# Kernel optimization log

Measured on AMD Instinct MI355X. Metric: run time of the kernel, lower is better.

## Reference

```python
import jax, jax.numpy as jnp
import numpy as np

NUM_HEADS = 8
N_WIN = 7
TOPK = 4


def _grid2seq(x, rs, m):
    # x: (B, C, H, W) -> (B, m, nregion, reg_size, head_dim)
    B, C, H, W = x.shape
    rh, rw = H // rs[0], W // rs[1]
    d = C // m
    x = x.reshape(B, m, d, rh, rs[0], rw, rs[1])
    x = jnp.einsum('bmdhpwq->bmhwpqd', x).reshape(B, m, rh * rw, rs[0] * rs[1], d)
    return x, rh, rw


def _seq2grid(x, rh, rw, rs):
    B, m, nreg, rsq, d = x.shape
    x = x.reshape(B, m, rh, rw, rs[0], rs[1], d)
    return jnp.einsum('bmhwpqd->bmdhpwq', x).reshape(B, m * d, rh * rs[0], rw * rs[1])


def setup_inputs() -> dict:
    key = jax.random.key(0)
    ks = jax.random.split(key, 7)
    C = 256
    inp = {
        'x': jax.random.normal(ks[0], (16, C, 56, 56), jnp.float32),
        'w_qkv': jax.random.normal(ks[1], (3 * C, C), jnp.float32) * 0.02,
        'b_qkv': jax.random.normal(ks[2], (3 * C,), jnp.float32) * 0.02,
        'w_lepe': jax.random.normal(ks[3], (C, 1, 3, 3), jnp.float32) * 0.02,
        'b_lepe': jax.random.normal(ks[4], (C,), jnp.float32) * 0.02,
        'w_out': jax.random.normal(ks[5], (C, C), jnp.float32) * 0.02,
        'b_out': jax.random.normal(ks[6], (C,), jnp.float32) * 0.02,
    }
    return inp


def reference(x, w_qkv, b_qkv, w_lepe, b_lepe, w_out, b_out):
    N, C, H, W = x.shape
    m = NUM_HEADS
    d = C // m
    scale = d ** (-0.5)
    rs = (max(1, H // N_WIN), max(1, W // N_WIN))  # (8, 8) here; H,W divisible -> no pad
    rh, rw = H // rs[0], W // rs[1]

    # 1x1 conv qkv projection
    qkv = jnp.einsum('nchw,oc->nohw', x, w_qkv) + b_qkv[None, :, None, None]
    q, k, v = jnp.split(qkv, 3, axis=1)

    # region-level routing (avg_pool over each region; exact divisibility -> plain mean)
    def region_mean(t):
        return t.reshape(N, C, rh, rs[0], rw, rs[1]).mean(axis=(3, 5))  # (N,C,rh,rw)

    q_r = jax.lax.stop_gradient(region_mean(q)).reshape(N, C, rh * rw).transpose(0, 2, 1)  # (N,nreg,C)
    k_r = jax.lax.stop_gradient(region_mean(k)).reshape(N, C, rh * rw)  # (N,C,nreg)
    a_r = q_r @ k_r  # (N, nreg, nreg)
    k_fixed = min(TOPK, a_r.shape[-1])
    _, idx_r = jax.lax.top_k(a_r, k_fixed)  # (N, nreg, topk)
    idx_r = jnp.broadcast_to(idx_r[:, None], (N, m, rh * rw, k_fixed))  # (N,m,nreg,topk)

    # token-level attention within routed regions
    q_seq, _, _ = _grid2seq(q, rs, m)  # (N,m,nreg,rs2,d)
    k_seq, _, _ = _grid2seq(k, rs, m)
    v_seq, _, _ = _grid2seq(v, rs, m)
    rs2 = k_seq.shape[-2]

    gather = jax.vmap(jax.vmap(lambda seq, i: seq[i]))  # over (batch, head)
    key_g = gather(k_seq, idx_r).reshape(N, m, rh * rw, k_fixed * rs2, d)
    val_g = gather(v_seq, idx_r).reshape(N, m, rh * rw, k_fixed * rs2, d)

    attn = jax.nn.softmax(jnp.einsum('bmnpd,bmnkd->bmnpk', q_seq * scale, key_g), axis=-1)
    out = jnp.einsum('bmnpk,bmnkd->bmnpd', attn, val_g)
    out = _seq2grid(out, rh, rw, rs)  # (N, C, H, W)

    # LEPE: depthwise 3x3 conv on v
    lepe = jax.lax.conv_general_dilated(
        v, w_lepe, window_strides=(1, 1), padding='SAME',
        feature_group_count=C, dimension_numbers=('NCHW', 'OIHW', 'NCHW'))
    out = out + lepe + b_lepe[None, :, None, None]

    # 1x1 conv output projection
    out = jnp.einsum('nchw,oc->nohw', out, w_out) + b_out[None, :, None, None]
    return out
```

## Files before the change

### kernel.cpp

```cpp
#include <hip/hip_runtime.h>
#include <cstdint>

#define DEV __device__ __forceinline__

using short8 = __attribute__((ext_vector_type(8))) short;
using f32x4  = __attribute__((ext_vector_type(4))) float;

#define MFMA __builtin_amdgcn_mfma_f32_16x16x32_bf16

DEV float bf2f(unsigned short u){
  union { unsigned int i; float f; } v; v.i = ((unsigned int)u) << 16; return v.f;
}
DEV unsigned short f2bf(float f){
  union { float f; unsigned int i; } v; v.f = f;
  unsigned int x = v.i;
  return (unsigned short)((x + 0x7fffu + ((x >> 16) & 1u)) >> 16);
}
DEV unsigned int cvtpk(float a, float b){
  unsigned int r;
  asm("v_cvt_pk_bf16_f32 %0, %1, %2" : "=v"(r) : "v"(a), "v"(b));
  return r;
}

__global__ __launch_bounds__(256) void k_prep(const float* __restrict__ w_qkv,
                                              const float* __restrict__ w_out,
                                              unsigned short* __restrict__ wqh_t,
                                              unsigned short* __restrict__ woh_t,
                                              unsigned short* __restrict__ wol_t){
  int i = blockIdx.x*256 + threadIdx.x;
  if (i < 196608){
    int o = i >> 8, c = i & 255, kc = c >> 5, kk = c & 31;
    wqh_t[kc*24576 + o*32 + kk] = f2bf(w_qkv[i]);
  } else {
    int j = i - 196608;
    if (j < 65536){
      int o = j >> 8, c = j & 255, kc = c >> 5, kk = c & 31;
      float v = w_out[j];
      unsigned short h = f2bf(v);
      int dst = kc*8192 + o*32 + kk;
      woh_t[dst] = h;
      wol_t[dst] = f2bf(v - bf2f(h));
    }
  }
}

__global__ __launch_bounds__(256) void k_xbar(const float* __restrict__ x,
                                              float* __restrict__ xbar){
  const int ry = blockIdx.x, n = blockIdx.y, cz = blockIdx.z;
  const int t = threadIdx.x, cg = t>>6, lane = t&63;
  for (int ci = 0; ci < 16; ++ci){
    int c = cz*64 + ci*4 + cg;
    const float* base = x + ((size_t)n*256 + c)*3136 + ry*8*56;
    float acc = 0.f;
    if (lane < 56){
      #pragma unroll
      for (int yy = 0; yy < 8; ++yy) acc += base[yy*56 + lane];
    }
    acc += __shfl_xor(acc, 1, 64);
    acc += __shfl_xor(acc, 2, 64);
    acc += __shfl_xor(acc, 4, 64);
    if ((lane&7) == 0 && lane < 56)
      xbar[((size_t)n*49 + ry*7 + (lane>>3))*256 + c] = acc * (1.0f/64.0f);
  }
}

__global__ __launch_bounds__(256) void k_qrkr(const float* __restrict__ xbar,
                                              const float* __restrict__ w_qkv,
                                              const float* __restrict__ b_qkv,
                                              float* __restrict__ q_r,
                                              float* __restrict__ k_r){
  __shared__ float4 xb4[448];
  const int wb = blockIdx.x, n = blockIdx.y, rz = blockIdx.z, t = threadIdx.x;
  {
    const float4* src = (const float4*)(xbar + (size_t)n*12544) + rz*448;
    for (int i = t; i < 448; i += 256) xb4[i] = src[i];
  }
  const int wrow = wb*64 + (t>>2), kl = t&3;
  float4 wreg[16];
  {
    const float4* wsrc = (const float4*)(w_qkv + (size_t)wrow*256) + kl*16;
    #pragma unroll
    for (int i = 0; i < 16; ++i) wreg[i] = wsrc[i];
  }
  __syncthreads();
  const float bias = b_qkv[wrow];
  for (int rl = 0; rl < 7; ++rl){
    float s = 0.f;
    #pragma unroll
    for (int i = 0; i < 16; ++i){
      float4 a = wreg[i], b = xb4[rl*64 + kl*16 + i];
      s += a.x*b.x + a.y*b.y + a.z*b.z + a.w*b.w;
    }
    s += __shfl_xor(s, 1, 64);
    s += __shfl_xor(s, 2, 64);
    if (kl == 0){
      int reg = rz*7 + rl;
      if (wrow < 256) q_r[((size_t)n*49 + reg)*256 + wrow] = s + bias;
      else            k_r[((size_t)n*49 + reg)*256 + wrow - 256] = s + bias;
    }
  }
}

__global__ __launch_bounds__(64) void k_topk(const float* __restrict__ q_r,
                                             const float* __restrict__ k_r,
                                             int* __restrict__ idx){
  __shared__ float sc[49];
  const int qreg = blockIdx.x, n = blockIdx.y, l = threadIdx.x;
  const float* qrow = q_r + ((size_t)n*49 + qreg)*256;
  const float q0 = qrow[l], q1 = qrow[l+64], q2 = qrow[l+128], q3 = qrow[l+192];
  for (int kr = 0; kr < 49; ++kr){
    const float* krow = k_r + ((size_t)n*49 + kr)*256;
    float s = q0*krow[l] + q1*krow[l+64] + q2*krow[l+128] + q3*krow[l+192];
    #pragma unroll
    for (int m = 1; m < 64; m <<= 1) s += __shfl_xor(s, m, 64);
    if (l == 0) sc[kr] = s;
  }
  __syncthreads();
  if (l == 0){
    #pragma unroll
    for (int s = 0; s < 4; ++s){
      float best = -3.4e38f; int bi = 0;
      for (int kr = 0; kr < 49; ++kr) if (sc[kr] > best){ best = sc[kr]; bi = kr; }
      idx[((size_t)n*49 + qreg)*4 + s] = bi;
      sc[bi] = -3.4e38f;
    }
  }
}

__global__ __launch_bounds__(256) void k_qkv(const float* __restrict__ x,
                                             const unsigned short* __restrict__ wqh_t,
                                             const float* __restrict__ b_qkv,
                                             unsigned short* __restrict__ q_rm,
                                             unsigned short* __restrict__ k_rm,
                                             unsigned short* __restrict__ v_t){
  __shared__ unsigned short xl[64*256];
  const int lin = blockIdx.x;
  const int xcd = lin & 7, jj = lin >> 3;
  const int jobid = xcd*294 + jj;
  const int z = jobid % 3;
  const int pair = jobid / 3;
  const int reg = pair % 49, n = pair / 49;

  const int ry = reg/7, rx = reg%7;
  const int t = threadIdx.x, w = t>>6, g = (t>>4)&3, c16 = t&15;
  {
    const int pq = (t & 15)*4, cc = t >> 4;
    const int row = pq >> 3, col = pq & 7;
    const float* src = x + ((size_t)n*256 + cc)*3136 + (ry*8 + row)*56 + rx*8 + col;
    for (int ci = 0; ci < 16; ++ci){
      float4 v4 = *reinterpret_cast<const float4*>(src + (size_t)ci*16*3136);
      int c = ci*16 + cc;
      xl[((pq+0)*256 + c) ^ (((pq+0)&15)<<3)] = f2bf(v4.x);
      xl[((pq+1)*256 + c) ^ (((pq+1)&15)<<3)] = f2bf(v4.y);
      xl[((pq+2)*256 + c) ^ (((pq+2)&15)<<3)] = f2bf(v4.z);
      xl[((pq+3)*256 + c) ^ (((pq+3)&15)<<3)] = f2bf(v4.w);
    }
  }
  __syncthreads();
  const size_t rb = (size_t)(n*8)*49 + reg;
  const int osw = w*16;

  if (z < 2){
    f32x4 acc[4][4] = {};
    for (int kc = 0; kc < 8; ++kc){
      short8 xf[4];
      #pragma unroll
      for (int pt = 0; pt < 4; ++pt){
        int p = pt*16 + c16;
        xf[pt] = *reinterpret_cast<const short8*>(&xl[(p*256 + kc*32 + 8*g) ^ ((p&15)<<3)]);
      }
      #pragma unroll
      for (int oi = 0; oi < 4; ++oi){
        const int os = z*256 + oi*64 + osw;
        short8 wf = *reinterpret_cast<const short8*>(wqh_t + (size_t)kc*24576 + (os + c16)*32 + 8*g);
        #pragma unroll
        for (int pt = 0; pt < 4; ++pt)
          acc[oi][pt] = MFMA(xf[pt], wf, acc[oi][pt], 0, 0, 0);
      }
    }
    #pragma unroll
    for (int oi = 0; oi < 4; ++oi){
      const int o = z*256 + oi*64 + osw + c16;
      const float bias = b_qkv[o];
      const int oc = o & 255, hh = oc >> 5, dd = oc & 31;
      unsigned short* dst = ((z == 0) ? q_rm : k_rm) + (rb + hh*49)*2048 + dd;
      #pragma unroll
      for (int pt = 0; pt < 4; ++pt)
        #pragma unroll
        for (int r = 0; r < 4; ++r){
          int tok = pt*16 + 4*g + r;
          dst[tok*32] = f2bf(acc[oi][pt][r] + bias);
        }
    }
  } else {
    f32x4 acc[4][4] = {};
    for (int kc = 0; kc < 8; ++kc){
      short8 xf[4];
      #pragma unroll
      for (int pt = 0; pt < 4; ++pt){
        int p = pt*16 + c16;
        xf[pt] = *reinterpret_cast<const short8*>(&xl[(p*256 + kc*32 + 8*g) ^ ((p&15)<<3)]);
      }
      #pragma unroll
      for (int oi = 0; oi < 4; ++oi){
        const int os = oi*64 + osw;
        short8 wf = *reinterpret_cast<const short8*>(wqh_t + (size_t)kc*24576 + (512 + os + c16)*32 + 8*g);
        #pragma unroll
        for (int pt = 0; pt < 4; ++pt)
          acc[oi][pt] = MFMA(wf, xf[pt], acc[oi][pt], 0, 0, 0);
      }
    }
    #pragma unroll
    for (int oi = 0; oi < 4; ++oi){
      #pragma unroll
      for (int r = 0; r < 4; ++r){
        int c = oi*64 + osw + 4*g + r;
        const float bias = b_qkv[512 + c];
        int hh = c >> 5, ch = c & 31;
        unsigned short* dst = v_t + (rb + hh*49)*2048 + ch*32;
        #pragma unroll
        for (int pt = 0; pt < 4; ++pt){
          int tok = pt*16 + c16;
          dst[(tok>>5)*1024 + (tok&31)] = f2bf(acc[oi][pt][r] + bias);
        }
      }
    }
  }
}

__global__ __launch_bounds__(256, 4) void k_attn(const unsigned short* __restrict__ q_rm,
                                                 const unsigned short* __restrict__ k_rm,
                                                 const unsigned short* __restrict__ v_t,
                                                 const int* __restrict__ idx,
                                                 const float* __restrict__ w_lepe,
                                                 const float* __restrict__ b_lepe,
                                                 unsigned short* __restrict__ att_hi,
                                                 unsigned short* __restrict__ att_lo){
  __shared__ unsigned short halo[10*320];
  __shared__ float wl_s[288];
  __shared__ float bl_s[32];

  const int lin = blockIdx.x + 49*(blockIdx.y + 8*blockIdx.z);
  const int xcd = lin & 7, j = lin >> 3;
  const int jq = j / 49;
  const int qreg = j - jq*49;
  const int hn = jq*8 + xcd;
  const int h = hn & 7, n = hn >> 3;

  const int t = threadIdx.x, w = t>>6, g = (t>>4)&3, c16 = t&15;
  const int ry = qreg/7, rx = qreg%7;
  const int gy0 = ry*8;

  int4 ridx = *reinterpret_cast<const int4*>(idx + ((size_t)n*49 + qreg)*4);
  int regs[4] = {ridx.x, ridx.y, ridx.z, ridx.w};

  const size_t hb = ((size_t)(n*8 + h))*49;

  wl_s[t < 288 ? t : 0] = w_lepe[h*288 + (t < 288 ? t : 0)];
  if (t < 32){
    wl_s[256 + t] = w_lepe[h*288 + 256 + t];
    bl_s[t] = b_lepe[h*32 + t];
  }
  #pragma unroll
  for (int pass = 0; pass < 2; ++pass){
    int s = pass ? (256 + t) : t;
    if (pass == 0 || t < 64){
      const int dy = s >> 5, c = s & 31;
      const int yy = gy0 + dy - 1;
      short8 inner = {0,0,0,0,0,0,0,0};
      unsigned short eL = 0, eR = 0;
      if (yy >= 0 && yy < 56){
        const int iry = yy >> 3, y7 = yy & 7;
        const size_t rowb = (size_t)(y7>>2)*1024 + c*32 + (y7&3)*8;
        inner = *reinterpret_cast<const short8*>(v_t + (hb + iry*7 + rx)*2048 + rowb);
        if (rx > 0) eL = v_t[(hb + iry*7 + rx - 1)*2048 + rowb + 7];
        if (rx < 6) eR = v_t[(hb + iry*7 + rx + 1)*2048 + rowb];
      }
      unsigned short* drow = &halo[dy*320 + c*10];
      drow[0] = eL;
      #pragma unroll
      for (int jj2 = 0; jj2 < 8; ++jj2) drow[1 + jj2] = (unsigned short)inner[jj2];
      drow[9] = eR;
    }
  }

  const int qtok = w*16 + c16;
  short8 qf = *reinterpret_cast<const short8*>(q_rm + (hb + qreg)*2048 + qtok*32 + 8*g);

  f32x4 s_acc[16];
  __builtin_amdgcn_s_setprio(1);
  #pragma unroll
  for (int f = 0; f < 16; ++f){
    const int tt = (f&3)*16 + c16;
    short8 kf = *reinterpret_cast<const short8*>(
        k_rm + (hb + regs[f>>2])*2048 + tt*32 + 8*g);
    f32x4 z = {0.f, 0.f, 0.f, 0.f};
    s_acc[f] = MFMA(kf, qf, z, 0, 0, 0);
  }
  __builtin_amdgcn_s_setprio(0);

  const float scale2 = 0.1767766952966369f * 1.4426950408889634f;
  float m = -3.4e38f;
  #pragma unroll
  for (int f = 0; f < 16; ++f)
    #pragma unroll
    for (int r = 0; r < 4; ++r) m = fmaxf(m, s_acc[f][r]);
  m = fmaxf(m, __shfl_xor(m, 16, 64));
  m = fmaxf(m, __shfl_xor(m, 32, 64));
  const float nms = -m*scale2;
  float su = 0.f;
  #pragma unroll
  for (int f = 0; f < 16; ++f)
    #pragma unroll
    for (int r = 0; r < 4; ++r){
      float e = exp2f(fmaf(s_acc[f][r], scale2, nms));
      s_acc[f][r] = e; su += e;
    }
  su += __shfl_xor(su, 16, 64);
  su += __shfl_xor(su, 32, 64);
  const float inv_lane = __builtin_amdgcn_rcpf(su);

  f32x4 oacc[2] = {};
  const int srcA = (t & 15) | ((t & 16) << 1);
  const int srcB = srcA + 16;
  const bool gsel = (t & 32) != 0;
  #pragma unroll
  for (int tc = 0; tc < 8; ++tc){
    const int fb = (tc>>1)*4 + (tc&1)*2;
    unsigned int a0 = cvtpk(s_acc[fb][0],   s_acc[fb][1]);
    unsigned int a1 = cvtpk(s_acc[fb][2],   s_acc[fb][3]);
    unsigned int b0 = cvtpk(s_acc[fb+1][0], s_acc[fb+1][1]);
    unsigned int b1 = cvtpk(s_acc[fb+1][2], s_acc[fb+1][3]);
    unsigned int wa0 = __shfl((int)a0, srcA, 64), wa1 = __shfl((int)a1, srcA, 64);
    unsigned int wa2 = __shfl((int)a0, srcB, 64), wa3 = __shfl((int)a1, srcB, 64);
    unsigned int wb0 = __shfl((int)b0, srcA, 64), wb1 = __shfl((int)b1, srcA, 64);
    unsigned int wb2 = __shfl((int)b0, srcB, 64), wb3 = __shfl((int)b1, srcB, 64);
    union { unsigned int u[4]; short8 s8; } pfu;
    pfu.u[0] = gsel ? wb0 : wa0;
    pfu.u[1] = gsel ? wb1 : wa1;
    pfu.u[2] = gsel ? wb2 : wa2;
    pfu.u[3] = gsel ? wb3 : wa3;
    const size_t vb = (hb + regs[tc>>1])*2048 + (tc&1)*1024 + 8*g;
    __builtin_amdgcn_s_setprio(1);
    #pragma unroll
    for (int dt = 0; dt < 2; ++dt){
      short8 vf = *reinterpret_cast<const short8*>(v_t + vb + (dt*16 + c16)*32);
      oacc[dt] = MFMA(pfu.s8, vf, oacc[dt], 0, 0, 0);
    }
    __builtin_amdgcn_s_setprio(0);
  }

  float invq[4];
  #pragma unroll
  for (int r = 0; r < 4; ++r)
    invq[r] = __shfl(inv_lane, 4*g + r, 64);

  __syncthreads();
  const int tok0 = w*16 + 4*g;
  const int ty = tok0>>3, tx0 = tok0&7;
  #pragma unroll
  for (int dt = 0; dt < 2; ++dt){
    const int cl = dt*16 + c16;
    float wl[9];
    #pragma unroll
    for (int kk = 0; kk < 9; ++kk) wl[kk] = wl_s[cl*9 + kk];
    const float bl = bl_s[cl];
    float vwin[3][6];
    #pragma unroll
    for (int dy = 0; dy < 3; ++dy){
      const unsigned short* hrow = &halo[(ty+dy)*320 + cl*10 + tx0];
      #pragma unroll
      for (int jj = 0; jj < 6; ++jj)
        vwin[dy][jj] = bf2f(hrow[jj]);
    }
    #pragma unroll
    for (int r = 0; r < 4; ++r){
      float a = fmaf(oacc[dt][r], invq[r], bl);
      #pragma unroll
      for (int dy = 0; dy < 3; ++dy)
        #pragma unroll
        for (int dx = 0; dx < 3; ++dx)
          a += wl[dy*3 + dx] * vwin[dy][r + dx];
      int tok = tok0 + r;
      size_t o = ((size_t)(n*49 + qreg)*8 + h)*2048 + tok*32 + dt*16 + c16;
      unsigned short hi = (unsigned short)cvtpk(a, a);
      att_hi[o] = hi;
      float alo = a - bf2f(hi);
      att_lo[o] = (unsigned short)cvtpk(alo, alo);
    }
  }
}

__global__ __launch_bounds__(512) void k_oproj(const unsigned short* __restrict__ ah_,
                                               const unsigned short* __restrict__ al_,
                                               const unsigned short* __restrict__ wh_t,
                                               const unsigned short* __restrict__ wl_t,
                                               const float* __restrict__ b_out,
                                               float* __restrict__ out){
  const int lin = blockIdx.x;
  const int jobid = (lin & 7)*98 + (lin >> 3);
  const int reg = jobid % 49, n = jobid / 49;
  const int t = threadIdx.x, w8 = t>>6, g = (t>>4)&3, c16 = t&15;
  const int ry = reg/7, rx = reg%7;
  const size_t abase = ((size_t)(n*49 + reg))*8*2048;
  const int os1 = w8*16, os2 = os1 + 128;
  f32x4 acc[2][4] = {};
  for (int kc = 0; kc < 8; ++kc){
    const size_t wb = (size_t)kc*8192 + 8*g;
    short8 wh1 = *reinterpret_cast<const short8*>(wh_t + wb + (os1 + c16)*32);
    short8 wl1 = *reinterpret_cast<const short8*>(wl_t + wb + (os1 + c16)*32);
    short8 wh2 = *reinterpret_cast<const short8*>(wh_t + wb + (os2 + c16)*32);
    short8 wl2 = *reinterpret_cast<const short8*>(wl_t + wb + (os2 + c16)*32);
    #pragma unroll
    for (int pt = 0; pt < 4; ++pt){
      size_t off = abase + (size_t)kc*2048 + (pt*16 + c16)*32 + 8*g;
      short8 xh = *reinterpret_cast<const short8*>(ah_ + off);
      short8 xl = *reinterpret_cast<const short8*>(al_ + off);
      acc[0][pt] = MFMA(wh1, xh, acc[0][pt], 0, 0, 0);
      acc[0][pt] = MFMA(wh1, xl, acc[0][pt], 0, 0, 0);
      acc[0][pt] = MFMA(wl1, xh, acc[0][pt], 0, 0, 0);
      acc[1][pt] = MFMA(wh2, xh, acc[1][pt], 0, 0, 0);
      acc[1][pt] = MFMA(wh2, xl, acc[1][pt], 0, 0, 0);
      acc[1][pt] = MFMA(wl2, xh, acc[1][pt], 0, 0, 0);
    }
  }
  #pragma unroll
  for (int s = 0; s < 2; ++s){
    const int os = s ? os2 : os1;
    #pragma unroll
    for (int r = 0; r < 4; ++r){
      int o = os + 4*g + r;
      float bias = b_out[o];
      #pragma unroll
      for (int pt = 0; pt < 4; ++pt){
        int tok = pt*16 + c16;
        int p = (ry*8 + (tok>>3))*56 + rx*8 + (tok&7);
        out[((size_t)n*256 + o)*3136 + p] = acc[s][pt][r] + bias;
      }
    }
  }
}

extern "C" void kernel_launch(void* const* d_in, const int* in_sizes, int n_in,
                              void* d_out, int out_size, void* d_ws, size_t ws_size,
                              hipStream_t stream){
  const float* x      = (const float*)d_in[0];
  const float* w_qkv  = (const float*)d_in[1];
  const float* b_qkv  = (const float*)d_in[2];
  const float* w_lepe = (const float*)d_in[3];
  const float* b_lepe = (const float*)d_in[4];
  const float* w_out  = (const float*)d_in[5];
  const float* b_out  = (const float*)d_in[6];
  float* out = (float*)d_out;

  char* ws = (char*)d_ws;
  size_t off = 0;
  auto take = [&](size_t bytes)->char*{
    char* p = ws + off; off += (bytes + 255) & ~(size_t)255; return p;
  };
  const size_t TEN = (size_t)16*3136*256*2;
  unsigned short* q_rm   = (unsigned short*)take(TEN);
  unsigned short* k_rm   = (unsigned short*)take(TEN);
  unsigned short* v_t    = (unsigned short*)take(TEN);
  unsigned short* att_hi = (unsigned short*)take(TEN);
  unsigned short* att_lo = (unsigned short*)take(TEN);
  float* xbar = (float*)take((size_t)16*49*256*4);
  float* q_r  = (float*)take((size_t)16*49*256*4);
  float* k_r  = (float*)take((size_t)16*49*256*4);
  int*   idxb = (int*)take((size_t)16*49*4*4);
  unsigned short* wqh_t = (unsigned short*)take((size_t)768*256*2);
  unsigned short* woh_t = (unsigned short*)take((size_t)256*256*2);
  unsigned short* wol_t = (unsigned short*)take((size_t)256*256*2);

  k_prep <<<dim3(1024), 256, 0, stream>>>(w_qkv, w_out, wqh_t, woh_t, wol_t);
  k_xbar <<<dim3(7, 16, 4), 256, 0, stream>>>(x, xbar);
  k_qrkr <<<dim3(8, 16, 7), 256, 0, stream>>>(xbar, w_qkv, b_qkv, q_r, k_r);
  k_topk <<<dim3(49, 16), 64, 0, stream>>>(q_r, k_r, idxb);
  k_qkv  <<<dim3(2352), 256, 0, stream>>>(x, wqh_t, b_qkv, q_rm, k_rm, v_t);
  k_attn <<<dim3(49, 8, 16), 256, 0, stream>>>(q_rm, k_rm, v_t, idxb, w_lepe, b_lepe, att_hi, att_lo);
  k_oproj<<<dim3(784), 512, 0, stream>>>(att_hi, att_lo, woh_t, wol_t, b_out, out);
}
```

Before: 248.9 us.

## Fuse routed attention and output projection into one kernel via LDS staging

Merges the attention+LEPE kernel and the output projection kernel into a single kernel that runs one block per (batch, region). Each of the 8 waves handles one head and loops over four query tiles. The hi/lo bf16 attention result is packed into shared memory and consumed directly by the projection MFMAs. This removes the global round trip of the att_hi/att_lo buffers and one kernel launch. In exchange the grid shrinks to 784 blocks with large LDS use (about 116KB) and a launch bound of one block per CU, which reduces occupancy and latency hiding.

After: 256.6 us. 1.03x slower.

```diff
diff --git a/kernel.cpp b/kernel.cpp
--- a/kernel.cpp
+++ b/kernel.cpp
@@ -228,182 +228,166 @@
   }
 }
 
-__global__ __launch_bounds__(256, 4) void k_attn(const unsigned short* __restrict__ q_rm,
-                                                 const unsigned short* __restrict__ k_rm,
-                                                 const unsigned short* __restrict__ v_t,
-                                                 const int* __restrict__ idx,
-                                                 const float* __restrict__ w_lepe,
-                                                 const float* __restrict__ b_lepe,
-                                                 unsigned short* __restrict__ att_hi,
-                                                 unsigned short* __restrict__ att_lo){
-  __shared__ unsigned short halo[10*320];
-  __shared__ float wl_s[288];
-  __shared__ float bl_s[32];
-
-  const int lin = blockIdx.x + 49*(blockIdx.y + 8*blockIdx.z);
-  const int xcd = lin & 7, j = lin >> 3;
-  const int jq = j / 49;
-  const int qreg = j - jq*49;
-  const int hn = jq*8 + xcd;
-  const int h = hn & 7, n = hn >> 3;
-
-  const int t = threadIdx.x, w = t>>6, g = (t>>4)&3, c16 = t&15;
-  const int ry = qreg/7, rx = qreg%7;
+__global__ __launch_bounds__(512, 1) void k_attnproj(
+    const unsigned short* __restrict__ q_rm,
+    const unsigned short* __restrict__ k_rm,
+    const unsigned short* __restrict__ v_t,
+    const int* __restrict__ idx,
+    const float* __restrict__ w_lepe,
+    const float* __restrict__ b_lepe,
+    const unsigned short* __restrict__ wh_t,
+    const unsigned short* __restrict__ wl_t,
+    const float* __restrict__ b_out,
+    float* __restrict__ out){
+  __shared__ unsigned int attP[64*257];
+  __shared__ unsigned short halo[8*3200];
+
+  const int lin = blockIdx.x;
+  const int jobid = (lin & 7)*98 + (lin >> 3);
+  const int reg = jobid % 49, n = jobid / 49;
+  const int t = threadIdx.x, h = t>>6, l = t&63, g = (l>>4)&3, c16 = l&15;
+  const int ry = reg/7, rx = reg%7;
   const int gy0 = ry*8;
 
-  int4 ridx = *reinterpret_cast<const int4*>(idx + ((size_t)n*49 + qreg)*4);
+  int4 ridx = *reinterpret_cast<const int4*>(idx + ((size_t)n*49 + reg)*4);
   int regs[4] = {ridx.x, ridx.y, ridx.z, ridx.w};
-
   const size_t hb = ((size_t)(n*8 + h))*49;
 
-  wl_s[t < 288 ? t : 0] = w_lepe[h*288 + (t < 288 ? t : 0)];
-  if (t < 32){
-    wl_s[256 + t] = w_lepe[h*288 + 256 + t];
-    bl_s[t] = b_lepe[h*32 + t];
-  }
   #pragma unroll
-  for (int pass = 0; pass < 2; ++pass){
-    int s = pass ? (256 + t) : t;
-    if (pass == 0 || t < 64){
-      const int dy = s >> 5, c = s & 31;
-      const int yy = gy0 + dy - 1;
-      short8 inner = {0,0,0,0,0,0,0,0};
-      unsigned short eL = 0, eR = 0;
-      if (yy >= 0 && yy < 56){
-        const int iry = yy >> 3, y7 = yy & 7;
-        const size_t rowb = (size_t)(y7>>2)*1024 + c*32 + (y7&3)*8;
-        inner = *reinterpret_cast<const short8*>(v_t + (hb + iry*7 + rx)*2048 + rowb);
-        if (rx > 0) eL = v_t[(hb + iry*7 + rx - 1)*2048 + rowb + 7];
-        if (rx < 6) eR = v_t[(hb + iry*7 + rx + 1)*2048 + rowb];
-      }
-      unsigned short* drow = &halo[dy*320 + c*10];
-      drow[0] = eL;
-      #pragma unroll
-      for (int jj2 = 0; jj2 < 8; ++jj2) drow[1 + jj2] = (unsigned short)inner[jj2];
-      drow[9] = eR;
-    }
-  }
-
-  const int qtok = w*16 + c16;
-  short8 qf = *reinterpret_cast<const short8*>(q_rm + (hb + qreg)*2048 + qtok*32 + 8*g);
-
-  f32x4 s_acc[16];
-  __builtin_amdgcn_s_setprio(1);
-  #pragma unroll
-  for (int f = 0; f < 16; ++f){
-    const int tt = (f&3)*16 + c16;
-    short8 kf = *reinterpret_cast<const short8*>(
-        k_rm + (hb + regs[f>>2])*2048 + tt*32 + 8*g);
-    f32x4 z = {0.f, 0.f, 0.f, 0.f};
-    s_acc[f] = MFMA(kf, qf, z, 0, 0, 0);
-  }
-  __builtin_amdgcn_s_setprio(0);
-
-  const float scale2 = 0.1767766952966369f * 1.4426950408889634f;
-  float m = -3.4e38f;
-  #pragma unroll
-  for (int f = 0; f < 16; ++f)
-    #pragma unroll
-    for (int r = 0; r < 4; ++r) m = fmaxf(m, s_acc[f][r]);
-  m = fmaxf(m, __shfl_xor(m, 16, 64));
-  m = fmaxf(m, __shfl_xor(m, 32, 64));
-  const float nms = -m*scale2;
-  float su = 0.f;
-  #pragma unroll
-  for (int f = 0; f < 16; ++f)
-    #pragma unroll
-    for (int r = 0; r < 4; ++r){
-      float e = exp2f(fmaf(s_acc[f][r], scale2, nms));
-      s_acc[f][r] = e; su += e;
-    }
-  su += __shfl_xor(su, 16, 64);
-  su += __shfl_xor(su, 32, 64);
-  const float inv_lane = __builtin_amdgcn_rcpf(su);
-
-  f32x4 oacc[2] = {};
-  const int srcA = (t & 15) | ((t & 16) << 1);
-  const int srcB = srcA + 16;
-  const bool gsel = (t & 32) != 0;
-  #pragma unroll
-  for (int tc = 0; tc < 8; ++tc){
-    const int fb = (tc>>1)*4 + (tc&1)*2;
-    unsigned int a0 = cvtpk(s_acc[fb][0],   s_acc[fb][1]);
-    unsigned int a1 = cvtpk(s_acc[fb][2],   s_acc[fb][3]);
-    unsigned int b0 = cvtpk(s_acc[fb+1][0], s_acc[fb+1][1]);
-    unsigned int b1 = cvtpk(s_acc[fb+1][2], s_acc[fb+1][3]);
-    unsigned int wa0 = __shfl((int)a0, srcA, 64), wa1 = __shfl((int)a1, srcA, 64);
-    unsigned int wa2 = __shfl((int)a0, srcB, 64), wa3 = __shfl((int)a1, srcB, 64);
-    unsigned int wb0 = __shfl((int)b0, srcA, 64), wb1 = __shfl((int)b1, srcA, 64);
-    unsigned int wb2 = __shfl((int)b0, srcB, 64), wb3 = __shfl((int)b1, srcB, 64);
-    union { unsigned int u[4]; short8 s8; } pfu;
-    pfu.u[0] = gsel ? wb0 : wa0;
-    pfu.u[1] = gsel ? wb1 : wa1;
-    pfu.u[2] = gsel ? wb2 : wa2;
-    pfu.u[3] = gsel ? wb3 : wa3;
-    const size_t vb = (hb + regs[tc>>1])*2048 + (tc&1)*1024 + 8*g;
-    __builtin_amdgcn_s_setprio(1);
-    #pragma unroll
-    for (int dt = 0; dt < 2; ++dt){
-      short8 vf = *reinterpret_cast<const short8*>(v_t + vb + (dt*16 + c16)*32);
-      oacc[dt] = MFMA(pfu.s8, vf, oacc[dt], 0, 0, 0);
-    }
-    __builtin_amdgcn_s_setprio(0);
-  }
-
-  float invq[4];
-  #pragma unroll
-  for (int r = 0; r < 4; ++r)
-    invq[r] = __shfl(inv_lane, 4*g + r, 64);
-
-  __syncthreads();
-  const int tok0 = w*16 + 4*g;
-  const int ty = tok0>>3, tx0 = tok0&7;
+  for (int it = 0; it < 5; ++it){
+    const int s = it*64 + l;
+    const int dy = s >> 5, c = s & 31;
+    const int yy = gy0 + dy - 1;
+    short8 inner = {0,0,0,0,0,0,0,0};
+    unsigned short eL = 0, eR = 0;
+    if (yy >= 0 && yy < 56){
+      const int iry = yy >> 3, y7 = yy & 7;
+      const size_t rowb = (size_t)(y7>>2)*1024 + c*32 + (y7&3)*8;
+      inner = *reinterpret_cast<const short8*>(v_t + (hb + iry*7 + rx)*2048 + rowb);
+      if (rx > 0) eL = v_t[(hb + iry*7 + rx - 1)*2048 + rowb + 7];
+      if (rx < 6) eR = v_t[(hb + iry*7 + rx + 1)*2048 + rowb];
+    }
+    unsigned short* drow = &halo[(h*10 + dy)*320 + c*10];
+    drow[0] = eL;
+    #pragma unroll
+    for (int jj2 = 0; jj2 < 8; ++jj2) drow[1 + jj2] = (unsigned short)inner[jj2];
+    drow[9] = eR;
+  }
+
+  float wl[2][9], blv[2];
   #pragma unroll
   for (int dt = 0; dt < 2; ++dt){
     const int cl = dt*16 + c16;
-    float wl[9];
-    #pragma unroll
-    for (int kk = 0; kk < 9; ++kk) wl[kk] = wl_s[cl*9 + kk];
-    const float bl = bl_s[cl];
-    float vwin[3][6];
-    #pragma unroll
-    for (int dy = 0; dy < 3; ++dy){
-      const unsigned short* hrow = &halo[(ty+dy)*320 + cl*10 + tx0];
-      #pragma unroll
-      for (int jj = 0; jj < 6; ++jj)
-        vwin[dy][jj] = bf2f(hrow[jj]);
-    }
-    #pragma unroll
-    for (int r = 0; r < 4; ++r){
-      float a = fmaf(oacc[dt][r], invq[r], bl);
-      #pragma unroll
-      for (int dy = 0; dy < 3; ++dy)
-        #pragma unroll
-        for (int dx = 0; dx < 3; ++dx)
-          a += wl[dy*3 + dx] * vwin[dy][r + dx];
-      int tok = tok0 + r;
-      size_t o = ((size_t)(n*49 + qreg)*8 + h)*2048 + tok*32 + dt*16 + c16;
-      unsigned short hi = (unsigned short)cvtpk(a, a);
-      att_hi[o] = hi;
-      float alo = a - bf2f(hi);
-      att_lo[o] = (unsigned short)cvtpk(alo, alo);
-    }
-  }
-}
-
-__global__ __launch_bounds__(512) void k_oproj(const unsigned short* __restrict__ ah_,
-                                               const unsigned short* __restrict__ al_,
-                                               const unsigned short* __restrict__ wh_t,
-                                               const unsigned short* __restrict__ wl_t,
-                                               const float* __restrict__ b_out,
-                                               float* __restrict__ out){
-  const int lin = blockIdx.x;
-  const int jobid = (lin & 7)*98 + (lin >> 3);
-  const int reg = jobid % 49, n = jobid / 49;
-  const int t = threadIdx.x, w8 = t>>6, g = (t>>4)&3, c16 = t&15;
-  const int ry = reg/7, rx = reg%7;
-  const size_t abase = ((size_t)(n*49 + reg))*8*2048;
-  const int os1 = w8*16, os2 = os1 + 128;
+    const float* wlp = w_lepe + ((size_t)h*32 + cl)*9;
+    #pragma unroll
+    for (int kk = 0; kk < 9; ++kk) wl[dt][kk] = wlp[kk];
+    blv[dt] = b_lepe[h*32 + cl];
+  }
+
+  asm volatile("s_waitcnt lgkmcnt(0)" ::: "memory");
+  __builtin_amdgcn_sched_barrier(0);
+
+  const float scale2 = 0.1767766952966369f * 1.4426950408889634f;
+  const int srcA = (l & 15) | ((l & 16) << 1);
+  const int srcB = srcA + 16;
+  const bool gsel = (l & 32) != 0;
+
+  for (int qt = 0; qt < 4; ++qt){
+    short8 qf = *reinterpret_cast<const short8*>(
+        q_rm + (hb + reg)*2048 + (qt*16 + c16)*32 + 8*g);
+
+    f32x4 s_acc[16];
+    #pragma unroll
+    for (int f = 0; f < 16; ++f){
+      const int tt = (f&3)*16 + c16;
+      short8 kf = *reinterpret_cast<const short8*>(
+          k_rm + (hb + regs[f>>2])*2048 + tt*32 + 8*g);
+      f32x4 z = {0.f, 0.f, 0.f, 0.f};
+      s_acc[f] = MFMA(kf, qf, z, 0, 0, 0);
+    }
+
+    float m = -3.4e38f;
+    #pragma unroll
+    for (int f = 0; f < 16; ++f)
+      #pragma unroll
+      for (int r = 0; r < 4; ++r) m = fmaxf(m, s_acc[f][r]);
+    m = fmaxf(m, __shfl_xor(m, 16, 64));
+    m = fmaxf(m, __shfl_xor(m, 32, 64));
+    const float nms = -m*scale2;
+    float su = 0.f;
+    #pragma unroll
+    for (int f = 0; f < 16; ++f)
+      #pragma unroll
+      for (int r = 0; r < 4; ++r){
+        float e = exp2f(fmaf(s_acc[f][r], scale2, nms));
+        s_acc[f][r] = e; su += e;
+      }
+    su += __shfl_xor(su, 16, 64);
+    su += __shfl_xor(su, 32, 64);
+    const float inv_lane = __builtin_amdgcn_rcpf(su);
+
+    f32x4 oacc[2] = {};
+    #pragma unroll
+    for (int tc = 0; tc < 8; ++tc){
+      const int fb = (tc>>1)*4 + (tc&1)*2;
+      unsigned int a0 = cvtpk(s_acc[fb][0],   s_acc[fb][1]);
+      unsigned int a1 = cvtpk(s_acc[fb][2],   s_acc[fb][3]);
+      unsigned int b0 = cvtpk(s_acc[fb+1][0], s_acc[fb+1][1]);
+      unsigned int b1 = cvtpk(s_acc[fb+1][2], s_acc[fb+1][3]);
+      unsigned int wa0 = __shfl((int)a0, srcA, 64), wa1 = __shfl((int)a1, srcA, 64);
+      unsigned int wa2 = __shfl((int)a0, srcB, 64), wa3 = __shfl((int)a1, srcB, 64);
+      unsigned int wb0 = __shfl((int)b0, srcA, 64), wb1 = __shfl((int)b1, srcA, 64);
+      unsigned int wb2 = __shfl((int)b0, srcB, 64), wb3 = __shfl((int)b1, srcB, 64);
+      union { unsigned int u[4]; short8 s8; } pfu;
+      pfu.u[0] = gsel ? wb0 : wa0;
+      pfu.u[1] = gsel ? wb1 : wa1;
+      pfu.u[2] = gsel ? wb2 : wa2;
+      pfu.u[3] = gsel ? wb3 : wa3;
+      const size_t vb = (hb + regs[tc>>1])*2048 + (tc&1)*1024 + 8*g;
+      #pragma unroll
+      for (int dt = 0; dt < 2; ++dt){
+        short8 vf = *reinterpret_cast<const short8*>(v_t + vb + (dt*16 + c16)*32);
+        oacc[dt] = MFMA(pfu.s8, vf, oacc[dt], 0, 0, 0);
+      }
+    }
+
+    float invq[4];
+    #pragma unroll
+    for (int r = 0; r < 4; ++r)
+      invq[r] = __shfl(inv_lane, 4*g + r, 64);
+
+    const int tok0 = qt*16 + 4*g;
+    const int ty = tok0>>3, tx0 = tok0&7;
+    #pragma unroll
+    for (int dt = 0; dt < 2; ++dt){
+      const int cl = dt*16 + c16;
+      float vwin[3][6];
+      #pragma unroll
+      for (int dy = 0; dy < 3; ++dy){
+        const unsigned short* hrow = &halo[(h*10 + ty + dy)*320 + cl*10 + tx0];
+        #pragma unroll
+        for (int jj = 0; jj < 6; ++jj)
+          vwin[dy][jj] = bf2f(hrow[jj]);
+      }
+      #pragma unroll
+      for (int r = 0; r < 4; ++r){
+        float a = fmaf(oacc[dt][r], invq[r], blv[dt]);
+        #pragma unroll
+        for (int dy = 0; dy < 3; ++dy)
+          #pragma unroll
+          for (int dx = 0; dx < 3; ++dx)
+            a += wl[dt][dy*3 + dx] * vwin[dy][r + dx];
+        unsigned int hp = cvtpk(a, a);
+        float lo = a - bf2f((unsigned short)hp);
+        attP[(tok0 + r)*257 + h*32 + dt*16 + c16] =
+            (hp & 0xffffu) | (cvtpk(lo, lo) << 16);
+      }
+    }
+  }
+
+  __syncthreads();
+
+  const int os1 = h*16, os2 = os1 + 128;
   f32x4 acc[2][4] = {};
   for (int kc = 0; kc < 8; ++kc){
     const size_t wb = (size_t)kc*8192 + 8*g;
@@ -413,15 +397,24 @@
     short8 wl2 = *reinterpret_cast<const short8*>(wl_t + wb + (os2 + c16)*32);
     #pragma unroll
     for (int pt = 0; pt < 4; ++pt){
-      size_t off = abase + (size_t)kc*2048 + (pt*16 + c16)*32 + 8*g;
-      short8 xh = *reinterpret_cast<const short8*>(ah_ + off);
-      short8 xl = *reinterpret_cast<const short8*>(al_ + off);
-      acc[0][pt] = MFMA(wh1, xh, acc[0][pt], 0, 0, 0);
-      acc[0][pt] = MFMA(wh1, xl, acc[0][pt], 0, 0, 0);
-      acc[0][pt] = MFMA(wl1, xh, acc[0][pt], 0, 0, 0);
-      acc[1][pt] = MFMA(wh2, xh, acc[1][pt], 0, 0, 0);
-      acc[1][pt] = MFMA(wh2, xl, acc[1][pt], 0, 0, 0);
-      acc[1][pt] = MFMA(wl2, xh, acc[1][pt], 0, 0, 0);
+      const unsigned int* ub = &attP[(pt*16 + c16)*257 + kc*32 + 8*g];
+      unsigned int u0 = ub[0], u1 = ub[1], u2 = ub[2], u3 = ub[3];
+      unsigned int u4 = ub[4], u5 = ub[5], u6 = ub[6], u7 = ub[7];
+      union { unsigned int u[4]; short8 s8; } xh, xl;
+      xh.u[0] = __builtin_amdgcn_perm(u1, u0, 0x05040100u);
+      xh.u[1] = __builtin_amdgcn_perm(u3, u2, 0x05040100u);
+      xh.u[2] = __builtin_amdgcn_perm(u5, u4, 0x05040100u);
+      xh.u[3] = __builtin_amdgcn_perm(u7, u6, 0x05040100u);
+      xl.u[0] = __builtin_amdgcn_perm(u1, u0, 0x07060302u);
+      xl.u[1] = __builtin_amdgcn_perm(u3, u2, 0x07060302u);
+      xl.u[2] = __builtin_amdgcn_perm(u5, u4, 0x07060302u);
+      xl.u[3] = __builtin_amdgcn_perm(u7, u6, 0x07060302u);
+      acc[0][pt] = MFMA(wh1, xh.s8, acc[0][pt], 0, 0, 0);
+      acc[0][pt] = MFMA(wh1, xl.s8, acc[0][pt], 0, 0, 0);
+      acc[0][pt] = MFMA(wl1, xh.s8, acc[0][pt], 0, 0, 0);
+      acc[1][pt] = MFMA(wh2, xh.s8, acc[1][pt], 0, 0, 0);
+      acc[1][pt] = MFMA(wh2, xl.s8, acc[1][pt], 0, 0, 0);
+      acc[1][pt] = MFMA(wl2, xh.s8, acc[1][pt], 0, 0, 0);
     }
   }
   #pragma unroll
@@ -462,8 +455,6 @@
   unsigned short* q_rm   = (unsigned short*)take(TEN);
   unsigned short* k_rm   = (unsigned short*)take(TEN);
   unsigned short* v_t    = (unsigned short*)take(TEN);
-  unsigned short* att_hi = (unsigned short*)take(TEN);
-  unsigned short* att_lo = (unsigned short*)take(TEN);
   float* xbar = (float*)take((size_t)16*49*256*4);
   float* q_r  = (float*)take((size_t)16*49*256*4);
   float* k_r  = (float*)take((size_t)16*49*256*4);
@@ -477,6 +468,6 @@
   k_qrkr <<<dim3(8, 16, 7), 256, 0, stream>>>(xbar, w_qkv, b_qkv, q_r, k_r);
   k_topk <<<dim3(49, 16), 64, 0, stream>>>(q_r, k_r, idxb);
   k_qkv  <<<dim3(2352), 256, 0, stream>>>(x, wqh_t, b_qkv, q_rm, k_rm, v_t);
-  k_attn <<<dim3(49, 8, 16), 256, 0, stream>>>(q_rm, k_rm, v_t, idxb, w_lepe, b_lepe, att_hi, att_lo);
-  k_oproj<<<dim3(784), 512, 0, stream>>>(att_hi, att_lo, woh_t, wol_t, b_out, out);
-}
+  k_attnproj<<<dim3(784), 512, 0, stream>>>(q_rm, k_rm, v_t, idxb, w_lepe, b_lepe,
+                                            woh_t, wol_t, b_out, out);
+}
```
